# Kernel optimization log

Hardware: AMD Instinct MI355X
Metric: run time of the kernel (lower is better)

## Reference

```python
import jax, jax.numpy as jnp
import numpy as np
import math

B, S, D, H, M, R = 4, 1024, 1024, 16, 4, 64
DH = D // H
EPS = 1e-8

def setup_inputs() -> dict:
    key = jax.random.key(0)
    ks = jax.random.split(key, 8)
    sc = 0.02
    return {
        'x': jax.random.normal(ks[0], (B, S, D), jnp.float32),
        'Wk': jax.random.normal(ks[1], (D, D), jnp.float32) * sc,
        'bk': jnp.zeros((D,), jnp.float32),
        'Wq': jax.random.normal(ks[2], (D, D), jnp.float32) * sc,
        'bq': jnp.zeros((D,), jnp.float32),
        'Wv': jax.random.normal(ks[3], (D, D), jnp.float32) * sc,
        'bv': jnp.zeros((D,), jnp.float32),
        'mask1': jax.random.normal(ks[4], (M, R, S), jnp.float32) * sc,
        'mask2': jax.random.normal(ks[5], (M, R, S), jnp.float32) * sc,
        'roll_back': jax.random.randint(ks[6], (M, S, S), 0, S, jnp.int64),
    }

def reference(x, Wk, bk, Wq, bq, Wv, bv, mask1, mask2, roll_back):
    def proj(W, b):
        # torch Linear: x @ W^T + b ; reshape to [B, H, S, DH]
        y = jnp.dot(x, W.T) + b
        return y.reshape(B, S, H, DH).transpose(0, 2, 1, 3)
    k = proj(Wk, bk)
    q = proj(Wq, bq)
    v = proj(Wv, bv)
    # learnable low-rank mask: [M, S, S]
    learnable_mask = jnp.einsum('mrs,mrt->mst', mask1, mask2)
    # gather along last dim with roll_back indices
    gathered = jnp.take_along_axis(learnable_mask, roll_back, axis=-1)  # [M, S, S]
    att = jnp.einsum('bhsd,bhtd->bhst', q, k) / math.sqrt(DH)  # [B, H, S, S]
    att = att.reshape(B, H // M, M, S, S) * gathered[None, None]
    att = att.reshape(B, H, S, S)
    # Frobenius norm over last two dims per (B, H)
    fro = jnp.sqrt(jnp.sum(att * att, axis=(-2, -1), keepdims=True))
    att = att / (fro + EPS)
    out = jnp.einsum('bhst,bhtd->bhsd', att, v)
    return out.transpose(0, 2, 1, 3).reshape(B, S, D)
```

## Files before the change

kernel.cpp:

```cpp
#include <hip/hip_runtime.h>
#include <hip/hip_bf16.h>
#include <stdint.h>

typedef __attribute__((ext_vector_type(8))) __bf16 bf16x8;
typedef __attribute__((ext_vector_type(4))) float  f32x4;
typedef __attribute__((ext_vector_type(16))) float f32x16;

__device__ __forceinline__ ushort f2bf(float f) {
    union { float f; uint32_t u; } v; v.f = f;
    uint32_t u = v.u;
    uint32_t r = 0x7FFFu + ((u >> 16) & 1u);
    return (ushort)((u + r) >> 16);
}
__device__ __forceinline__ float bf2f(ushort u) {
    union { uint32_t u; float f; } v; v.u = ((uint32_t)u) << 16;
    return v.f;
}

typedef __attribute__((address_space(3))) uint32_t lds_u32_t;
typedef const __attribute__((address_space(1))) uint32_t glb_u32_t;
__device__ __forceinline__ void async_copy16(const void* g, void* l) {
    __builtin_amdgcn_global_load_lds((glb_u32_t*)g, (lds_u32_t*)l, 16, 0, 0);
}

__global__ __launch_bounds__(256) void convert_all(
    const float* __restrict__ x, const float* __restrict__ wk,
    const float* __restrict__ wq, const float* __restrict__ wv,
    ushort* __restrict__ xb, ushort* __restrict__ wball)
{
    int i = blockIdx.x * 256 + threadIdx.x;
    const float* src; ushort* dst; int j;
    if (i < 1048576) { src = x; dst = xb; j = i; }
    else {
        int t = i - 1048576;
        int z = t >> 18;
        j = t & 262143;
        src = (z == 0) ? wk : (z == 1) ? wq : wv;
        dst = wball + z * 1048576;
    }
    float4 f = ((const float4*)src)[j];
    ushort4 o;
    o.x = f2bf(f.x); o.y = f2bf(f.y); o.z = f2bf(f.z); o.w = f2bf(f.w);
    ((ushort4*)dst)[j] = o;
}

__global__ __launch_bounds__(256) void proj_gemm(
    const ushort* __restrict__ xb, const ushort* __restrict__ wball,
    const float* __restrict__ bk, const float* __restrict__ bq, const float* __restrict__ bv,
    ushort* __restrict__ kd, ushort* __restrict__ qd, ushort* __restrict__ vd)
{
    __shared__ ushort As[3 * 128 * 32];
    __shared__ ushort Bs[3 * 128 * 32];
    const int z = blockIdx.z;
    const int row0 = blockIdx.x * 128;
    const int col0 = blockIdx.y * 128;
    const ushort* wb = wball + z * 1048576;
    const int tid = threadIdx.x;
    const int lane = tid & 63, wave = tid >> 6;
    const int quad = lane >> 4, m15 = lane & 15;
    const int wr = wave >> 1, wc = wave & 1;

    f32x4 acc[4][4];
    for (int i = 0; i < 4; i++)
        for (int j = 0; j < 4; j++) acc[i][j] = (f32x4){0.f, 0.f, 0.f, 0.f};

#define STAGE(BI, KK) do {                                                        \
        _Pragma("unroll")                                                         \
        for (int i_ = 0; i_ < 2; i_++) {                                          \
            int c_ = tid + i_ * 256;                                  \
            int r_ = c_ >> 2, cjp_ = c_ & 3;                                      \
            int cj_ = cjp_ ^ ((r_ >> 1) & 3);                                     \
            async_copy16(&xb[(row0 + r_) * 1024 + (KK) + cj_ * 8],                \
                         &As[(BI) * 4096 + c_ * 8]);                              \
            async_copy16(&wb[(col0 + r_) * 1024 + (KK) + cj_ * 8],                \
                         &Bs[(BI) * 4096 + c_ * 8]);                              \
        }                                                                         \
    } while (0)

#define COMPUTE(BI) do {                                                          \
        const ushort* a_ = &As[(BI) * 4096];                                      \
        const ushort* b_ = &Bs[(BI) * 4096];                                      \
        bf16x8 af[4], bfv[4];                                                     \
        _Pragma("unroll")                                                         \
        for (int fr = 0; fr < 4; fr++) {                                          \
            int row = wr * 64 + fr * 16 + m15;                                    \
            af[fr] = *(const bf16x8*)&a_[row * 32 + ((quad ^ ((row >> 1) & 3)) * 8)]; \
        }                                                                         \
        _Pragma("unroll")                                                         \
        for (int fc = 0; fc < 4; fc++) {                                          \
            int row = wc * 64 + fc * 16 + m15;                                    \
            bfv[fc] = *(const bf16x8*)&b_[row * 32 + ((quad ^ ((row >> 1) & 3)) * 8)]; \
        }                                                                         \
        _Pragma("unroll")                                                         \
        for (int fr = 0; fr < 4; fr++)                                            \
            _Pragma("unroll")                                                     \
            for (int fc = 0; fc < 4; fc++)                                        \
                acc[fr][fc] = __builtin_amdgcn_mfma_f32_16x16x32_bf16(            \
                    af[fr], bfv[fc], acc[fr][fc], 0, 0, 0);                       \
    } while (0)

    STAGE(0, 0);
    STAGE(1, 32);

    int cur = 0;
    #pragma unroll 3
    for (int t = 0; t < 30; ++t) {
        int sb = cur + 2; if (sb >= 3) sb -= 3;
        STAGE(sb, (t + 2) * 32);
        asm volatile("s_waitcnt vmcnt(8)" ::: "memory");
        __builtin_amdgcn_s_barrier();
        COMPUTE(cur);
        __builtin_amdgcn_s_barrier();
        cur = (cur == 2) ? 0 : cur + 1;
    }
    asm volatile("s_waitcnt vmcnt(4)" ::: "memory");
    __builtin_amdgcn_s_barrier();
    COMPUTE(cur);
    cur = (cur == 2) ? 0 : cur + 1;
    asm volatile("s_waitcnt vmcnt(0)" ::: "memory");
    __builtin_amdgcn_s_barrier();
    COMPUTE(cur);

#undef STAGE
#undef COMPUTE

    const float* bias = (z == 0) ? bk : (z == 1) ? bq : bv;
    ushort* dstA = (z == 0) ? kd : qd;
    for (int fr = 0; fr < 4; fr++) {
        int ibase = row0 + wr * 64 + fr * 16 + quad * 4;
        int b_ = ibase >> 10, s = ibase & 1023;
        for (int fc = 0; fc < 4; fc++) {
            int j = col0 + wc * 64 + fc * 16 + m15;
            int h = j >> 6, dh = j & 63;
            float bb = bias[j];
            if (z < 2) {
                for (int r = 0; r < 4; r++)
                    dstA[((b_ * 16 + h) * 1024 + (s + r)) * 64 + dh] = f2bf(acc[fr][fc][r] + bb);
            } else {
                ushort4 o;
                o.x = f2bf(acc[fr][fc][0] + bb);
                o.y = f2bf(acc[fr][fc][1] + bb);
                o.z = f2bf(acc[fr][fc][2] + bb);
                o.w = f2bf(acc[fr][fc][3] + bb);
                *(ushort4*)&vd[((b_ * 16 + h) * 64 + dh) * 1024 + s] = o;
            }
        }
    }
}

__global__ __launch_bounds__(256) void mask_fused(
    const float* __restrict__ m1, const float* __restrict__ m2,
    const int* __restrict__ rb, ushort* __restrict__ gth)
{
    __shared__ float As8[64 * 8];
    __shared__ float lmS[8 * 1024];
    const int s0 = blockIdx.x * 8;
    const int m = blockIdx.y;
    const int tid = threadIdx.x;

    if (tid < 128) {
        int r = tid >> 1, half = tid & 1;
        *(float4*)&As8[r * 8 + half * 4] =
            *(const float4*)&m1[(m * 64 + r) * 1024 + s0 + half * 4];
    }
    __syncthreads();

    f32x4 acc8[8];
    #pragma unroll
    for (int s = 0; s < 8; s++) acc8[s] = (f32x4){0.f, 0.f, 0.f, 0.f};
    const float* m2b = m2 + m * 65536 + tid * 4;
    #pragma unroll 4
    for (int r = 0; r < 64; r++) {
        float4 b4 = *(const float4*)&m2b[r * 1024];
        f32x4 b = (f32x4){b4.x, b4.y, b4.z, b4.w};
        #pragma unroll
        for (int s = 0; s < 8; s++) {
            float a = As8[r * 8 + s];
            acc8[s] += a * b;
        }
    }
    #pragma unroll
    for (int s = 0; s < 8; s++)
        *(f32x4*)&lmS[s * 1024 + tid * 4] = acc8[s];
    __syncthreads();

    const int base = (m * 1024 + s0) * 1024;
    #pragma unroll
    for (int i = 0; i < 8; i++) {
        int c = tid + i * 256;
        int row = c >> 8, j = (c & 255) * 4;
        int4 idx = *(const int4*)&rb[base + row * 1024 + j];
        ushort4 o;
        o.x = f2bf(lmS[row * 1024 + (idx.x & 1023)] * 0.125f);
        o.y = f2bf(lmS[row * 1024 + (idx.y & 1023)] * 0.125f);
        o.z = f2bf(lmS[row * 1024 + (idx.z & 1023)] * 0.125f);
        o.w = f2bf(lmS[row * 1024 + (idx.w & 1023)] * 0.125f);
        *(ushort4*)&gth[base + row * 1024 + j] = o;
    }
}

__global__ __launch_bounds__(256, 4) void attention(
    const ushort* __restrict__ qd, const ushort* __restrict__ kd, const ushort* __restrict__ vd,
    const ushort* __restrict__ gth, float* __restrict__ O, float* __restrict__ ss)
{
    __shared__ ushort Ks[64 * 72];
    __shared__ ushort Vs[64 * 72];
    __shared__ ushort Ps[64 * 72];
    __shared__ float red[4];
    const int s0 = blockIdx.x * 64;
    const int bh = blockIdx.y;
    const int mm = bh & 3;
    const int tid = threadIdx.x, lane = tid & 63, wave = tid >> 6;
    const int l31 = lane & 31, hl = lane >> 5;
    const int wr2 = wave >> 1, wc2 = wave & 1;

    const int r0_ = tid >> 3,          o0_ = (tid & 7) * 8;
    const int r1_ = (tid + 256) >> 3,  o1_ = ((tid + 256) & 7) * 8;

    const ushort* kdb = kd + bh * 65536;
    const ushort* vdb = vd + bh * 65536;

    const int srow = wr2 * 32 + l31;
    const int tb   = wc2 * 32 + 4 * hl;
    const ushort* grow = gth + mm * 1048576 + (s0 + srow) * 1024 + tb;

    *(uint4*)&Ks[r0_ * 72 + o0_] = *(const uint4*)&qd[(bh * 1024 + s0 + r0_) * 64 + o0_];
    *(uint4*)&Ks[r1_ * 72 + o1_] = *(const uint4*)&qd[(bh * 1024 + s0 + r1_) * 64 + o1_];
    uint4 kr0 = *(const uint4*)&kdb[r0_ * 64 + o0_];
    uint4 kr1 = *(const uint4*)&kdb[r1_ * 64 + o1_];
    uint4 vr0 = *(const uint4*)&vdb[r0_ * 1024 + o0_];
    uint4 vr1 = *(const uint4*)&vdb[r1_ * 1024 + o1_];
    ushort4 mk0 = *(const ushort4*)&grow[0];
    ushort4 mk1 = *(const ushort4*)&grow[8];
    ushort4 mk2 = *(const ushort4*)&grow[16];
    ushort4 mk3 = *(const ushort4*)&grow[24];
    __syncthreads();
    bf16x8 qf[4];
    #pragma unroll
    for (int kk = 0; kk < 4; kk++)
        qf[kk] = *(const bf16x8*)&Ks[srow * 72 + kk * 16 + hl * 8];
    __syncthreads();

    *(uint4*)&Ks[r0_ * 72 + o0_] = kr0;
    *(uint4*)&Ks[r1_ * 72 + o1_] = kr1;
    *(uint4*)&Vs[r0_ * 72 + o0_] = vr0;
    *(uint4*)&Vs[r1_ * 72 + o1_] = vr1;
    kr0 = *(const uint4*)&kdb[(64 + r0_) * 64 + o0_];
    kr1 = *(const uint4*)&kdb[(64 + r1_) * 64 + o1_];
    vr0 = *(const uint4*)&vdb[r0_ * 1024 + 64 + o0_];
    vr1 = *(const uint4*)&vdb[r1_ * 1024 + 64 + o1_];
    __syncthreads();

    f32x16 oacc;
    #pragma unroll
    for (int i = 0; i < 16; i++) oacc[i] = 0.f;
    float ss0 = 0.f, ss1 = 0.f, ss2 = 0.f, ss3 = 0.f;

    for (int t = 0; t < 16; ++t) {
        f32x16 p;
        #pragma unroll
        for (int i = 0; i < 16; i++) p[i] = 0.f;
        #pragma unroll
        for (int kk = 0; kk < 4; kk++) {
            bf16x8 kf = *(const bf16x8*)&Ks[(wc2 * 32 + l31) * 72 + kk * 16 + hl * 8];
            p = __builtin_amdgcn_mfma_f32_32x32x16_bf16(kf, qf[kk], p, 0, 0, 0);
        }
#define MBLK(G, MK) do {                                               \
            float pv0 = p[4*(G)+0] * bf2f((MK).x);                     \
            float pv1 = p[4*(G)+1] * bf2f((MK).y);                     \
            float pv2 = p[4*(G)+2] * bf2f((MK).z);                     \
            float pv3 = p[4*(G)+3] * bf2f((MK).w);                     \
            ss0 += pv0 * pv0; ss1 += pv1 * pv1;                        \
            ss2 += pv2 * pv2; ss3 += pv3 * pv3;                        \
            ushort4 o_;                                                \
            o_.x = f2bf(pv0); o_.y = f2bf(pv1);                        \
            o_.z = f2bf(pv2); o_.w = f2bf(pv3);                        \
            *(ushort4*)&Ps[srow * 72 + tb + 8 * (G)] = o_;             \
        } while (0)
        MBLK(0, mk0); MBLK(1, mk1); MBLK(2, mk2); MBLK(3, mk3);
#undef MBLK
        if (t < 15) {
            const ushort* gn = grow + (t + 1) * 64;
            mk0 = *(const ushort4*)&gn[0];
            mk1 = *(const ushort4*)&gn[8];
            mk2 = *(const ushort4*)&gn[16];
            mk3 = *(const ushort4*)&gn[24];
        }
        __syncthreads();
        #pragma unroll
        for (int kk = 0; kk < 4; kk++) {
            bf16x8 a = *(const bf16x8*)&Ps[(wr2 * 32 + l31) * 72 + kk * 16 + hl * 8];
            bf16x8 b = *(const bf16x8*)&Vs[(wc2 * 32 + l31) * 72 + kk * 16 + hl * 8];
            oacc = __builtin_amdgcn_mfma_f32_32x32x16_bf16(a, b, oacc, 0, 0, 0);
        }
        __syncthreads();
        if (t < 15) {
            *(uint4*)&Ks[r0_ * 72 + o0_] = kr0;
            *(uint4*)&Ks[r1_ * 72 + o1_] = kr1;
            *(uint4*)&Vs[r0_ * 72 + o0_] = vr0;
            *(uint4*)&Vs[r1_ * 72 + o1_] = vr1;
            if (t < 14) {
                const int tn = (t + 2) * 64;
                kr0 = *(const uint4*)&kdb[(tn + r0_) * 64 + o0_];
                kr1 = *(const uint4*)&kdb[(tn + r1_) * 64 + o1_];
                vr0 = *(const uint4*)&vdb[r0_ * 1024 + tn + o0_];
                vr1 = *(const uint4*)&vdb[r1_ * 1024 + tn + o1_];
            }
            __syncthreads();
        }
    }
    #pragma unroll
    for (int reg = 0; reg < 16; reg++) {
        int s = s0 + wr2 * 32 + (reg & 3) + 8 * (reg >> 2) + 4 * hl;
        int dh = wc2 * 32 + l31;
        O[(bh * 1024 + s) * 64 + dh] = oacc[reg];
    }
    float ssacc = (ss0 + ss1) + (ss2 + ss3);
    for (int off = 32; off; off >>= 1) ssacc += __shfl_down(ssacc, off, 64);
    if (lane == 0) red[wave] = ssacc;
    __syncthreads();
    if (tid == 0) atomicAdd(&ss[bh], red[0] + red[1] + red[2] + red[3]);
}

__global__ __launch_bounds__(256) void normalize_out(const float* __restrict__ O,
                                                     const float* __restrict__ ss,
                                                     float* __restrict__ out)
{
    int gid = blockIdx.x * 256 + threadIdx.x;
    int e = gid * 4;
    int bh = e >> 16;
    float inv = 1.f / (sqrtf(ss[bh]) + 1e-8f);
    float4 v4 = *(const float4*)&O[e];
    int b_ = bh >> 4, h = bh & 15;
    int s = (e >> 6) & 1023, dh = e & 63;
    float4 o4 = {v4.x * inv, v4.y * inv, v4.z * inv, v4.w * inv};
    *(float4*)&out[((b_ * 1024 + s) * 16 + h) * 64 + dh] = o4;
}

extern "C" void kernel_launch(void* const* d_in, const int* in_sizes, int n_in,
                              void* d_out, int out_size, void* d_ws, size_t ws_size,
                              hipStream_t stream) {
    const float* x  = (const float*)d_in[0];
    const float* Wk = (const float*)d_in[1];
    const float* bk = (const float*)d_in[2];
    const float* Wq = (const float*)d_in[3];
    const float* bq = (const float*)d_in[4];
    const float* Wv = (const float*)d_in[5];
    const float* bv = (const float*)d_in[6];
    const float* m1 = (const float*)d_in[7];
    const float* m2 = (const float*)d_in[8];
    const int*   rb = (const int*)d_in[9];
    float* out = (float*)d_out;

    char* ws = (char*)d_ws;
    ushort* xb    = (ushort*)(ws);
    ushort* wball = (ushort*)(ws + 8388608);
    ushort* kd    = (ushort*)(ws + 14680064);
    ushort* qd    = (ushort*)(ws + 23068672);
    ushort* vd    = (ushort*)(ws + 31457280);
    float*  O     = (float*)(ws + 39845888);
    ushort* gth   = (ushort*)(ws + 56623104);
    float*  ssb   = (float*)(ws + 65011712);

    convert_all<<<7168, 256, 0, stream>>>(x, Wk, Wq, Wv, xb, wball);
    proj_gemm<<<dim3(32, 8, 3), 256, 0, stream>>>(xb, wball, bk, bq, bv, kd, qd, vd);
    mask_fused<<<dim3(128, 4), 256, 0, stream>>>(m1, m2, rb, gth);
    hipMemsetAsync(ssb, 0, 64 * sizeof(float), stream);
    attention<<<dim3(16, 64), 256, 0, stream>>>(qd, kd, vd, gth, O, ssb);
    normalize_out<<<4096, 256, 0, stream>>>(O, ssb, out);
}
```

Baseline: 195.9 us.

## Stage gathered mask tiles through LDS and swizzle P writes to avoid bank conflicts

The gathered mask tile is now loaded with coalesced 16-byte global reads into a padded LDS buffer, prefetched two tiles ahead alongside K/V, instead of strided 8-byte per-lane global loads each iteration. Each thread reads its mask values from LDS. P tile writes and reads use an XOR swizzle on 4-element chunks to reduce LDS bank conflicts. This adds LDS usage and extra LDS traffic, which may affect occupancy.

```diff
diff --git a/kernel.cpp b/kernel.cpp
--- a/kernel.cpp
+++ b/kernel.cpp
@@ -206,6 +206,7 @@
     __shared__ ushort Ks[64 * 72];
     __shared__ ushort Vs[64 * 72];
     __shared__ ushort Ps[64 * 72];
+    __shared__ ushort Ms[64 * 76];
     __shared__ float red[4];
     const int s0 = blockIdx.x * 64;
     const int bh = blockIdx.y;
@@ -219,10 +220,11 @@
 
     const ushort* kdb = kd + bh * 65536;
     const ushort* vdb = vd + bh * 65536;
+    const ushort* gbase = gth + mm * 1048576 + s0 * 1024;
 
     const int srow = wr2 * 32 + l31;
     const int tb   = wc2 * 32 + 4 * hl;
-    const ushort* grow = gth + mm * 1048576 + (s0 + srow) * 1024 + tb;
+    const int f_   = (srow >> 3) & 1;
 
     *(uint4*)&Ks[r0_ * 72 + o0_] = *(const uint4*)&qd[(bh * 1024 + s0 + r0_) * 64 + o0_];
     *(uint4*)&Ks[r1_ * 72 + o1_] = *(const uint4*)&qd[(bh * 1024 + s0 + r1_) * 64 + o1_];
@@ -230,10 +232,8 @@
     uint4 kr1 = *(const uint4*)&kdb[r1_ * 64 + o1_];
     uint4 vr0 = *(const uint4*)&vdb[r0_ * 1024 + o0_];
     uint4 vr1 = *(const uint4*)&vdb[r1_ * 1024 + o1_];
-    ushort4 mk0 = *(const ushort4*)&grow[0];
-    ushort4 mk1 = *(const ushort4*)&grow[8];
-    ushort4 mk2 = *(const ushort4*)&grow[16];
-    ushort4 mk3 = *(const ushort4*)&grow[24];
+    uint4 mr0 = *(const uint4*)&gbase[r0_ * 1024 + o0_];
+    uint4 mr1 = *(const uint4*)&gbase[r1_ * 1024 + o1_];
     __syncthreads();
     bf16x8 qf[4];
     #pragma unroll
@@ -245,10 +245,16 @@
     *(uint4*)&Ks[r1_ * 72 + o1_] = kr1;
     *(uint4*)&Vs[r0_ * 72 + o0_] = vr0;
     *(uint4*)&Vs[r1_ * 72 + o1_] = vr1;
+    *(uint2*)&Ms[r0_ * 76 + o0_]     = make_uint2(mr0.x, mr0.y);
+    *(uint2*)&Ms[r0_ * 76 + o0_ + 4] = make_uint2(mr0.z, mr0.w);
+    *(uint2*)&Ms[r1_ * 76 + o1_]     = make_uint2(mr1.x, mr1.y);
+    *(uint2*)&Ms[r1_ * 76 + o1_ + 4] = make_uint2(mr1.z, mr1.w);
     kr0 = *(const uint4*)&kdb[(64 + r0_) * 64 + o0_];
     kr1 = *(const uint4*)&kdb[(64 + r1_) * 64 + o1_];
     vr0 = *(const uint4*)&vdb[r0_ * 1024 + 64 + o0_];
     vr1 = *(const uint4*)&vdb[r1_ * 1024 + 64 + o1_];
+    mr0 = *(const uint4*)&gbase[r0_ * 1024 + 64 + o0_];
+    mr1 = *(const uint4*)&gbase[r1_ * 1024 + 64 + o1_];
     __syncthreads();
 
     f32x16 oacc;
@@ -265,33 +271,30 @@
             bf16x8 kf = *(const bf16x8*)&Ks[(wc2 * 32 + l31) * 72 + kk * 16 + hl * 8];
             p = __builtin_amdgcn_mfma_f32_32x32x16_bf16(kf, qf[kk], p, 0, 0, 0);
         }
-#define MBLK(G, MK) do {                                               \
-            float pv0 = p[4*(G)+0] * bf2f((MK).x);                     \
-            float pv1 = p[4*(G)+1] * bf2f((MK).y);                     \
-            float pv2 = p[4*(G)+2] * bf2f((MK).z);                     \
-            float pv3 = p[4*(G)+3] * bf2f((MK).w);                     \
-            ss0 += pv0 * pv0; ss1 += pv1 * pv1;                        \
-            ss2 += pv2 * pv2; ss3 += pv3 * pv3;                        \
-            ushort4 o_;                                                \
-            o_.x = f2bf(pv0); o_.y = f2bf(pv1);                        \
-            o_.z = f2bf(pv2); o_.w = f2bf(pv3);                        \
-            *(ushort4*)&Ps[srow * 72 + tb + 8 * (G)] = o_;             \
-        } while (0)
-        MBLK(0, mk0); MBLK(1, mk1); MBLK(2, mk2); MBLK(3, mk3);
-#undef MBLK
-        if (t < 15) {
-            const ushort* gn = grow + (t + 1) * 64;
-            mk0 = *(const ushort4*)&gn[0];
-            mk1 = *(const ushort4*)&gn[8];
-            mk2 = *(const ushort4*)&gn[16];
-            mk3 = *(const ushort4*)&gn[24];
+        #pragma unroll
+        for (int g = 0; g < 4; g++) {
+            ushort4 mk = *(const ushort4*)&Ms[srow * 76 + tb + 8 * g];
+            float pv0 = p[4 * g + 0] * bf2f(mk.x);
+            float pv1 = p[4 * g + 1] * bf2f(mk.y);
+            float pv2 = p[4 * g + 2] * bf2f(mk.z);
+            float pv3 = p[4 * g + 3] * bf2f(mk.w);
+            ss0 += pv0 * pv0; ss1 += pv1 * pv1;
+            ss2 += pv2 * pv2; ss3 += pv3 * pv3;
+            ushort4 o_;
+            o_.x = f2bf(pv0); o_.y = f2bf(pv1);
+            o_.z = f2bf(pv2); o_.w = f2bf(pv3);
+            int u_ = (wc2 * 8 + hl + 2 * g) ^ f_;
+            *(ushort4*)&Ps[srow * 72 + u_ * 4] = o_;
         }
         __syncthreads();
         #pragma unroll
         for (int kk = 0; kk < 4; kk++) {
-            bf16x8 a = *(const bf16x8*)&Ps[(wr2 * 32 + l31) * 72 + kk * 16 + hl * 8];
+            int m2 = kk * 4 + hl * 2;
+            union { uint2 u2[2]; bf16x8 v; } av;
+            av.u2[0] = *(const uint2*)&Ps[srow * 72 + ((m2 ^ f_) * 4)];
+            av.u2[1] = *(const uint2*)&Ps[srow * 72 + (((m2 + 1) ^ f_) * 4)];
             bf16x8 b = *(const bf16x8*)&Vs[(wc2 * 32 + l31) * 72 + kk * 16 + hl * 8];
-            oacc = __builtin_amdgcn_mfma_f32_32x32x16_bf16(a, b, oacc, 0, 0, 0);
+            oacc = __builtin_amdgcn_mfma_f32_32x32x16_bf16(av.v, b, oacc, 0, 0, 0);
         }
         __syncthreads();
         if (t < 15) {
@@ -299,12 +302,18 @@
             *(uint4*)&Ks[r1_ * 72 + o1_] = kr1;
             *(uint4*)&Vs[r0_ * 72 + o0_] = vr0;
             *(uint4*)&Vs[r1_ * 72 + o1_] = vr1;
+            *(uint2*)&Ms[r0_ * 76 + o0_]     = make_uint2(mr0.x, mr0.y);
+            *(uint2*)&Ms[r0_ * 76 + o0_ + 4] = make_uint2(mr0.z, mr0.w);
+            *(uint2*)&Ms[r1_ * 76 + o1_]     = make_uint2(mr1.x, mr1.y);
+            *(uint2*)&Ms[r1_ * 76 + o1_ + 4] = make_uint2(mr1.z, mr1.w);
             if (t < 14) {
                 const int tn = (t + 2) * 64;
                 kr0 = *(const uint4*)&kdb[(tn + r0_) * 64 + o0_];
                 kr1 = *(const uint4*)&kdb[(tn + r1_) * 64 + o1_];
                 vr0 = *(const uint4*)&vdb[r0_ * 1024 + tn + o0_];
                 vr1 = *(const uint4*)&vdb[r1_ * 1024 + tn + o1_];
+                mr0 = *(const uint4*)&gbase[r0_ * 1024 + tn + o0_];
+                mr1 = *(const uint4*)&gbase[r1_ * 1024 + tn + o1_];
             }
             __syncthreads();
         }
```

Result: no change. 193.0 us (-1.5%).
